# Kernel optimization log

Hardware: AMD Instinct MI355X
Metric: run time of the kernel (lower is better)

The kernel has to match this reference:

```python
import jax, jax.numpy as jnp
import numpy as np
from jax import lax

B_J0 = 0.01   # config.b_j0
R_M = 1.0     # config.R_m
BETA = 1.8    # isAdapt=1 branch
GAMMA = 0.5   # config.gamma
LENS = 0.5    # config.lens
SCALE = 6.0   # config.scale
HIGHT = 0.15  # config.hight


def _gauss(x, mu, sigma):
    return jnp.exp(-(x - mu) ** 2 / (2.0 * sigma ** 2)) / jnp.sqrt(2.0 * jnp.pi) / sigma


@jax.custom_vjp
def spike_fn(x):
    return (x > 0).astype(x.dtype)

def _spike_fwd(x):
    return spike_fn(x), x

def _spike_bwd(x, g):
    # 'MG' multi-gaussian surrogate gradient from ActFun_adp.backward
    temp = (_gauss(x, 0.0, LENS) * (1.0 + HIGHT)
            - _gauss(x, LENS, SCALE * LENS) * HIGHT
            - _gauss(x, -LENS, SCALE * LENS) * HIGHT)
    return (g * temp * GAMMA,)

spike_fn.defvjp(_spike_fwd, _spike_bwd)


def setup_inputs() -> dict:
    key = jax.random.key(0)
    ks = jax.random.split(key, 20)
    B, T, I, H, O = 256, 250, 700, 128, 20
    def xav(k, shape):
        lim = jnp.sqrt(6.0 / (shape[0] + shape[1]))
        return jax.random.uniform(k, shape, jnp.float32, -lim, lim)
    def orth(k, n):
        a = jax.random.normal(k, (n, n), jnp.float32)
        q, r = jnp.linalg.qr(a)
        return q * jnp.sign(jnp.diag(r))[None, :]
    return {
        'input': jax.random.normal(ks[0], (B, T, I), jnp.float32),
        'A1_mask': jnp.ones((H, H), jnp.float32),
        'A2_mask': jnp.ones((H, H), jnp.float32),
        'W_ih1': xav(ks[1], (H, I)), 'b_ih1': jnp.zeros((H,), jnp.float32),
        'W_h1h1': orth(ks[2], H), 'b_h1h1': jnp.zeros((H,), jnp.float32),
        'W_h1h2': xav(ks[3], (H, H)), 'b_h1h2': jnp.zeros((H,), jnp.float32),
        'W_h2h2': orth(ks[4], H), 'b_h2h2': jnp.zeros((H,), jnp.float32),
        'W_h2o': xav(ks[5], (O, H)), 'b_h2o': jnp.zeros((O,), jnp.float32),
        'tau_adp_h1': 150.0 + 10.0 * jax.random.normal(ks[6], (H,), jnp.float32),
        'tau_adp_h2': 150.0 + 10.0 * jax.random.normal(ks[7], (H,), jnp.float32),
        'tau_m_h1': 20.0 + 5.0 * jax.random.normal(ks[8], (H,), jnp.float32),
        'tau_m_h2': 20.0 + 5.0 * jax.random.normal(ks[9], (H,), jnp.float32),
        'tau_m_o': 20.0 + 5.0 * jax.random.normal(ks[10], (O,), jnp.float32),
        'hid1_mem0': jax.random.uniform(ks[11], (B, H), jnp.float32),
        'hid2_mem0': jax.random.uniform(ks[12], (B, H), jnp.float32),
        'out_mem0': jax.random.uniform(ks[13], (B, O), jnp.float32),
    }


def reference(input, A1_mask, A2_mask,
              W_ih1, b_ih1, W_h1h1, b_h1h1, W_h1h2, b_h1h2,
              W_h2h2, b_h2h2, W_h2o, b_h2o,
              tau_adp_h1, tau_adp_h2, tau_m_h1, tau_m_h2, tau_m_o,
              hid1_mem0, hid2_mem0, out_mem0):
    B, T, _ = input.shape
    H = W_ih1.shape[0]
    O = W_h2o.shape[0]
    # time-constant decays (dt = 1), computed once
    a1 = jnp.exp(-1.0 / tau_m_h1)
    r1 = jnp.exp(-1.0 / tau_adp_h1)
    a2 = jnp.exp(-1.0 / tau_m_h2)
    r2 = jnp.exp(-1.0 / tau_adp_h2)
    ao = jnp.exp(-1.0 / tau_m_o)

    xT = jnp.swapaxes(input, 0, 1)  # [T, B, I]
    carry0 = (hid1_mem0, jnp.zeros((B, H), input.dtype), jnp.full((B, H), B_J0, input.dtype),
              hid2_mem0, jnp.zeros((B, H), input.dtype), jnp.full((B, H), B_J0, input.dtype),
              out_mem0, jnp.zeros((B, O), input.dtype))

    def step(carry, xs):
        x_t, t = xs
        h1m, h1s, b1, h2m, h2s, b2, om, acc = carry
        # layer 1: input + recurrent drive, adaptive threshold LIF update
        in1 = x_t @ W_ih1.T + b_ih1 + h1s @ W_h1h1.T + b_h1h1
        b1 = r1 * b1 + (1.0 - r1) * h1s
        Bth1 = B_J0 + BETA * b1
        h1m = h1m * a1 + (1.0 - a1) * R_M * in1 - Bth1 * h1s
        h1s = spike_fn(h1m - Bth1)
        # layer 2
        in2 = h1s @ W_h1h2.T + b_h1h2 + h2s @ W_h2h2.T + b_h2h2
        b2 = r2 * b2 + (1.0 - r2) * h2s
        Bth2 = B_J0 + BETA * b2
        h2m = h2m * a2 + (1.0 - a2) * R_M * in2 - Bth2 * h2s
        h2s = spike_fn(h2m - Bth2)
        # leaky-integrator readout (no spike)
        om = om * ao + (1.0 - ao) * R_M * (h2s @ W_h2o.T + b_h2o)
        # accumulate softmax only for t > 10
        acc = acc + jnp.where(t > 10, 1.0, 0.0) * jax.nn.softmax(om, axis=1)
        return (h1m, h1s, b1, h2m, h2s, b2, om, acc), None

    final, _ = lax.scan(step, carry0, (xT, jnp.arange(T)))
    output = final[-1]
    A_norm = jnp.sum(jnp.abs(W_h1h1)) + jnp.sum(jnp.abs(W_h2h2))
    return output, A_norm


if __name__ == '__main__':
    out = reference(**setup_inputs())
    print(out[0].shape, out[1])
```

## Files before the change

### kernel.cpp

```cpp
#include <hip/hip_runtime.h>
#include <hip/hip_bf16.h>
#include <stdint.h>

#define HN 128
#define TSTEPS 250
#define ON 20
#define GK 700
#define NKT 22
#define KS 4
#define NSLOT 63

typedef _Float16 h2 __attribute__((ext_vector_type(2)));
typedef _Float16 h8 __attribute__((ext_vector_type(8)));
typedef float f4 __attribute__((ext_vector_type(4)));

__device__ __forceinline__ uint32_t pack2u(float x, float y) {
    h2 p; p.x = (_Float16)x; p.y = (_Float16)y;
    return __builtin_bit_cast(uint32_t, p);
}

__global__ __launch_bounds__(256) void ff_gemm(const float* __restrict__ X,
                                               const float* __restrict__ W,
                                               const float* __restrict__ bias,
                                               float* __restrict__ out) {
    __shared__ __align__(16) uint32_t Xs[2][128][16];
    __shared__ __align__(16) uint32_t Ws[2][128][16];
    const int tid   = threadIdx.x;
    const int w     = tid >> 6;
    const int lane  = tid & 63;
    const int m0    = blockIdx.x * 128;
    const int srow  = tid & 127;
    const int shalf = tid >> 7;
    const int lr    = lane & 15;
    const int lg    = lane >> 4;

    f4 acc[2][8];
#pragma unroll
    for (int m = 0; m < 2; ++m)
#pragma unroll
        for (int n = 0; n < 8; ++n) acc[m][n] = (f4){0.f, 0.f, 0.f, 0.f};

    float4 x4[4], w4[4];

#define LOADT(t)                                                               \
    {                                                                          \
        const int k0 = (t) * 32 + shalf * 16;                                  \
        if ((t) < 21 || shalf == 0) {                                          \
            _Pragma("unroll")                                                  \
            for (int q = 0; q < 4; ++q) {                                      \
                x4[q] = *(const float4*)&X[(size_t)(m0 + srow) * GK + k0 + q * 4]; \
                w4[q] = *(const float4*)&W[(size_t)srow * GK + k0 + q * 4];    \
            }                                                                  \
        } else {                                                               \
            _Pragma("unroll")                                                  \
            for (int q = 0; q < 3; ++q) {                                      \
                x4[q] = *(const float4*)&X[(size_t)(m0 + srow) * GK + k0 + q * 4]; \
                w4[q] = *(const float4*)&W[(size_t)srow * GK + k0 + q * 4];    \
            }                                                                  \
            x4[3] = (float4){0.f, 0.f, 0.f, 0.f};                              \
            w4[3] = (float4){0.f, 0.f, 0.f, 0.f};                              \
        }                                                                      \
    }
#define STORET(buf)                                                            \
    {                                                                          \
        _Pragma("unroll")                                                      \
        for (int q = 0; q < 4; ++q) {                                          \
            Xs[buf][srow][shalf * 8 + 2 * q]     = pack2u(x4[q].x, x4[q].y);   \
            Xs[buf][srow][shalf * 8 + 2 * q + 1] = pack2u(x4[q].z, x4[q].w);   \
            Ws[buf][srow][shalf * 8 + 2 * q]     = pack2u(w4[q].x, w4[q].y);   \
            Ws[buf][srow][shalf * 8 + 2 * q + 1] = pack2u(w4[q].z, w4[q].w);   \
        }                                                                      \
    }

    LOADT(0);
    STORET(0);
    __syncthreads();
    int cur = 0;
    for (int t = 0; t < NKT; ++t) {
        if (t + 1 < NKT) LOADT(t + 1);
        h8 a[2];
#pragma unroll
        for (int m = 0; m < 2; ++m) {
            const uint4 au = *(const uint4*)&Xs[cur][w * 32 + m * 16 + lr][lg * 4];
            a[m] = __builtin_bit_cast(h8, au);
        }
#pragma unroll
        for (int n = 0; n < 8; ++n) {
            const uint4 bu = *(const uint4*)&Ws[cur][n * 16 + lr][lg * 4];
            const h8 bf = __builtin_bit_cast(h8, bu);
            acc[0][n] = __builtin_amdgcn_mfma_f32_16x16x32_f16(a[0], bf, acc[0][n], 0, 0, 0);
            acc[1][n] = __builtin_amdgcn_mfma_f32_16x16x32_f16(a[1], bf, acc[1][n], 0, 0, 0);
        }
        if (t + 1 < NKT) STORET(cur ^ 1);
        __syncthreads();
        cur ^= 1;
    }

    float bv[8];
#pragma unroll
    for (int n = 0; n < 8; ++n) bv[n] = bias[n * 16 + lr];
#pragma unroll
    for (int m = 0; m < 2; ++m)
#pragma unroll
        for (int q = 0; q < 4; ++q) {
            const size_t row = (size_t)(m0 + w * 32 + m * 16 + lg * 4 + q);
#pragma unroll
            for (int n = 0; n < 8; ++n)
                out[row * HN + n * 16 + lr] = acc[m][n][q] + bv[n];
        }
#undef LOADT
#undef STORET
}

__device__ __forceinline__ void qrow(const float* __restrict__ src,
                                     uint4 (&wq)[8], float& sc) {
    float amax = 0.f;
#pragma unroll
    for (int q = 0; q < 32; ++q) {
        float4 v = *(const float4*)&src[q * 4];
        amax = fmaxf(amax, fmaxf(fmaxf(fabsf(v.x), fabsf(v.y)),
                                 fmaxf(fabsf(v.z), fabsf(v.w))));
    }
    const float qs = (amax > 0.f) ? 127.f / amax : 0.f;
#pragma unroll
    for (int g = 0; g < 8; ++g) {
        uint32_t u[4];
#pragma unroll
        for (int e = 0; e < 4; ++e) {
            float4 v = *(const float4*)&src[g * 16 + e * 4];
            const int q0 = (int)rintf(v.x * qs), q1 = (int)rintf(v.y * qs);
            const int q2 = (int)rintf(v.z * qs), q3 = (int)rintf(v.w * qs);
            u[e] = (uint32_t)(q0 & 255) | ((uint32_t)(q1 & 255) << 8) |
                   ((uint32_t)(q2 & 255) << 16) | ((uint32_t)(q3 & 255) << 24);
        }
        wq[g].x = u[0]; wq[g].y = u[1]; wq[g].z = u[2]; wq[g].w = u[3];
    }
    sc = (amax > 0.f) ? amax / 127.f : 0.f;
}

__device__ __forceinline__ int mvqr(const uint4 (&wq)[8], const uint4 (&sv)[8]) {
    int a0 = 0, a1 = 0, a2 = 0, a3 = 0;
#pragma unroll
    for (int g = 0; g < 8; ++g) {
        a0 = __builtin_amdgcn_sdot4((int)wq[g].x, (int)sv[g].x, a0, false);
        a1 = __builtin_amdgcn_sdot4((int)wq[g].y, (int)sv[g].y, a1, false);
        a2 = __builtin_amdgcn_sdot4((int)wq[g].z, (int)sv[g].z, a2, false);
        a3 = __builtin_amdgcn_sdot4((int)wq[g].w, (int)sv[g].w, a3, false);
    }
    return (a0 + a1) + (a2 + a3);
}

#define LOADQP(ptr, sv)                                                        \
    {                                                                          \
        const uint4* _p = (const uint4*)(ptr);                                 \
        _Pragma("unroll") for (int _g = 0; _g < 8; ++_g) sv[_g] = _p[_g];      \
    }

__device__ __forceinline__ uint32_t nib2bytes(uint32_t nib) {
    return ((nib & 15u) * 0x00204081u) & 0x01010101u;
}

__device__ __forceinline__ void spread_masks(unsigned long long lo,
                                             unsigned long long hi,
                                             uint4 (&sv)[8]) {
#pragma unroll
    for (int g = 0; g < 8; ++g) {
        const unsigned long long src = (g < 4) ? lo : hi;
        const int base = (g & 3) * 16;
        sv[g].x = nib2bytes((uint32_t)(src >> (base + 0)));
        sv[g].y = nib2bytes((uint32_t)(src >> (base + 4)));
        sv[g].z = nib2bytes((uint32_t)(src >> (base + 8)));
        sv[g].w = nib2bytes((uint32_t)(src >> (base + 12)));
    }
}

__global__ __launch_bounds__(320) void srnn_pipe13(
    const float* __restrict__ ff,
    const float* __restrict__ W_h1h1, const float* __restrict__ b_h1h1,
    const float* __restrict__ W_h1h2, const float* __restrict__ b_h1h2,
    const float* __restrict__ W_h2h2, const float* __restrict__ b_h2h2,
    const float* __restrict__ W_h2o,  const float* __restrict__ b_h2o,
    const float* __restrict__ tau_adp_h1, const float* __restrict__ tau_adp_h2,
    const float* __restrict__ tau_m_h1,   const float* __restrict__ tau_m_h2,
    const float* __restrict__ tau_m_o,
    const float* __restrict__ h1m0, const float* __restrict__ h2m0,
    const float* __restrict__ om0,
    float* __restrict__ out) {
    const int b    = blockIdx.x;
    const int tid  = threadIdx.x;
    const int w    = tid >> 6;
    const int lane = tid & 63;

    __shared__ __align__(16) uint32_t s1buf[2][KS][32];
    __shared__ __align__(16) uint32_t s2buf[2][KS][32];
    __shared__ __align__(16) float    pbbuf[2][KS][HN];
    __shared__ __align__(16) float    rdbuf[2][KS][32];

    if (w == 0) {
        const int jl = lane, jh = lane + 64;
        uint4 wql[8], wqh[8]; float sAl, sAh;
        qrow(W_h1h1 + jl * HN, wql, sAl);
        qrow(W_h1h1 + jh * HN, wqh, sAh);
        float h1m_l = h1m0[b * HN + jl], h1m_h = h1m0[b * HN + jh];
        const float a1l = expf(-1.f / tau_m_h1[jl]), a1h = expf(-1.f / tau_m_h1[jh]);
        const float r1l = expf(-1.f / tau_adp_h1[jl]), r1h = expf(-1.f / tau_adp_h1[jh]);
        const float bil = b_h1h1[jl], bih = b_h1h1[jh];
        float b1l = 0.01f, b1h = 0.01f, s1l = 0.f, s1h = 0.f;
        const float* fpl = ff + (size_t)b * TSTEPS * HN + jl;
        const float* fph = ff + (size_t)b * TSTEPS * HN + jh;
        float fcl[KS], fch[KS];
#pragma unroll
        for (int k = 0; k < KS; ++k) {
            fcl[k] = fpl[(size_t)k * HN];
            fch[k] = fph[(size_t)k * HN];
        }
        unsigned long long mklo = 0ull, mkhi = 0ull;
        for (int s = 0; s < NSLOT + 4; ++s) {
            float fnl[KS], fnh[KS];
#pragma unroll
            for (int k = 0; k < KS; ++k) {
                const int t = KS * (s + 1) + k;
                fnl[k] = (t < TSTEPS) ? fpl[(size_t)t * HN] : 0.f;
                fnh[k] = (t < TSTEPS) ? fph[(size_t)t * HN] : 0.f;
            }
            if (s < NSLOT) {
#pragma unroll
                for (int k = 0; k < KS; ++k) {
                    const int t = KS * s + k;
                    if (t < TSTEPS) {
                        uint4 sv[8];
                        spread_masks(mklo, mkhi, sv);
                        const float pAl = sAl * (float)mvqr(wql, sv);
                        const float pAh = sAh * (float)mvqr(wqh, sv);
                        b1l = r1l * b1l + (1.f - r1l) * s1l;
                        b1h = r1h * b1h + (1.f - r1h) * s1h;
                        const float Btl = 0.01f + 1.8f * b1l;
                        const float Bth = 0.01f + 1.8f * b1h;
                        h1m_l = h1m_l * a1l + (1.f - a1l) * (fcl[k] + bil + pAl) - Btl * s1l;
                        h1m_h = h1m_h * a1h + (1.f - a1h) * (fch[k] + bih + pAh) - Bth * s1h;
                        const int spl = (h1m_l - Btl > 0.f) ? 1 : 0;
                        const int sph = (h1m_h - Bth > 0.f) ? 1 : 0;
                        s1l = (float)spl; s1h = (float)sph;
                        mklo = __ballot(spl); mkhi = __ballot(sph);
                        if (lane < 32) {
                            const unsigned long long src = (lane < 16) ? mklo : mkhi;
                            s1buf[s & 1][k][lane] =
                                nib2bytes((uint32_t)(src >> ((lane & 15) * 4)));
                        }
                    }
                }
            }
#pragma unroll
            for (int k = 0; k < KS; ++k) { fcl[k] = fnl[k]; fch[k] = fnh[k]; }
            __syncthreads();
        }
    } else if (w == 1) {
        const int jl = lane, jh = lane + 64;
        uint4 wql[8], wqh[8]; float sBl, sBh;
        qrow(W_h1h2 + jl * HN, wql, sBl);
        qrow(W_h1h2 + jh * HN, wqh, sBh);
        for (int s = 0; s < NSLOT + 4; ++s) {
            if (s >= 1 && s - 1 < NSLOT) {
#pragma unroll
                for (int k = 0; k < KS; ++k) {
                    const int t = KS * (s - 1) + k;
                    if (t < TSTEPS) {
                        uint4 sv[8];
                        LOADQP(&s1buf[(s - 1) & 1][k][0], sv);
                        pbbuf[s & 1][k][jl] = sBl * (float)mvqr(wql, sv);
                        pbbuf[s & 1][k][jh] = sBh * (float)mvqr(wqh, sv);
                    }
                }
            }
            __syncthreads();
        }
    } else if (w == 2) {
        const int jl = lane, jh = lane + 64;
        uint4 wql[8], wqh[8]; float sCl, sCh;
        qrow(W_h2h2 + jl * HN, wql, sCl);
        qrow(W_h2h2 + jh * HN, wqh, sCh);
        float h2m_l = h2m0[b * HN + jl], h2m_h = h2m0[b * HN + jh];
        const float a2l = expf(-1.f / tau_m_h2[jl]), a2h = expf(-1.f / tau_m_h2[jh]);
        const float r2l = expf(-1.f / tau_adp_h2[jl]), r2h = expf(-1.f / tau_adp_h2[jh]);
        const float bil = b_h1h2[jl] + b_h2h2[jl];
        const float bih = b_h1h2[jh] + b_h2h2[jh];
        float b2l = 0.01f, b2h = 0.01f, s2l = 0.f, s2h = 0.f;
        unsigned long long mklo = 0ull, mkhi = 0ull;
        for (int s = 0; s < NSLOT + 4; ++s) {
            if (s >= 2 && s - 2 < NSLOT) {
#pragma unroll
                for (int k = 0; k < KS; ++k) {
                    const int t = KS * (s - 2) + k;
                    if (t < TSTEPS) {
                        uint4 sv[8];
                        spread_masks(mklo, mkhi, sv);
                        const float pCl = sCl * (float)mvqr(wql, sv);
                        const float pCh = sCh * (float)mvqr(wqh, sv);
                        const float pBl = pbbuf[(s - 1) & 1][k][jl];
                        const float pBh = pbbuf[(s - 1) & 1][k][jh];
                        b2l = r2l * b2l + (1.f - r2l) * s2l;
                        b2h = r2h * b2h + (1.f - r2h) * s2h;
                        const float Btl = 0.01f + 1.8f * b2l;
                        const float Bth = 0.01f + 1.8f * b2h;
                        h2m_l = h2m_l * a2l + (1.f - a2l) * (pBl + pCl + bil) - Btl * s2l;
                        h2m_h = h2m_h * a2h + (1.f - a2h) * (pBh + pCh + bih) - Bth * s2h;
                        const int spl = (h2m_l - Btl > 0.f) ? 1 : 0;
                        const int sph = (h2m_h - Bth > 0.f) ? 1 : 0;
                        s2l = (float)spl; s2h = (float)sph;
                        mklo = __ballot(spl); mkhi = __ballot(sph);
                        if (lane < 32) {
                            const unsigned long long src = (lane < 16) ? mklo : mkhi;
                            s2buf[s & 1][k][lane] =
                                nib2bytes((uint32_t)(src >> ((lane & 15) * 4)));
                        }
                    }
                }
            }
            __syncthreads();
        }
    } else if (w == 3) {
        const int o = lane;
        uint4 wq[8]; float sO;
        qrow(W_h2o + (size_t)((o < ON) ? o : 0) * HN, wq, sO);
        if (o >= ON) sO = 0.f;
        for (int s = 0; s < NSLOT + 4; ++s) {
            if (s >= 3 && s - 3 < NSLOT) {
#pragma unroll
                for (int k = 0; k < KS; ++k) {
                    const int t = KS * (s - 3) + k;
                    if (t < TSTEPS) {
                        uint4 sv[8];
                        LOADQP(&s2buf[(s - 1) & 1][k][0], sv);
                        if (o < 32) rdbuf[s & 1][k][o] = sO * (float)mvqr(wq, sv);
                    }
                }
            }
            __syncthreads();
        }
    } else {
        float omv[ON], accv[ON], aov[ON], bov[ON];
#pragma unroll
        for (int k = 0; k < ON; ++k) {
            omv[k]  = om0[b * ON + k];
            aov[k]  = expf(-1.f / tau_m_o[k]);
            bov[k]  = b_h2o[k];
            accv[k] = 0.f;
        }
        for (int s = 0; s < NSLOT + 4; ++s) {
            if (s >= 4 && s - 4 < NSLOT) {
#pragma unroll
                for (int kk = 0; kk < KS; ++kk) {
                    const int t = KS * (s - 4) + kk;
                    if (t < TSTEPS) {
                        const float4* rp = (const float4*)&rdbuf[(s - 1) & 1][kk][0];
                        const float4 r0 = rp[0], r1 = rp[1], r2 = rp[2],
                                     r3 = rp[3], r4 = rp[4];
                        float rd[ON];
                        rd[0] = r0.x;  rd[1] = r0.y;  rd[2] = r0.z;  rd[3] = r0.w;
                        rd[4] = r1.x;  rd[5] = r1.y;  rd[6] = r1.z;  rd[7] = r1.w;
                        rd[8] = r2.x;  rd[9] = r2.y;  rd[10] = r2.z; rd[11] = r2.w;
                        rd[12] = r3.x; rd[13] = r3.y; rd[14] = r3.z; rd[15] = r3.w;
                        rd[16] = r4.x; rd[17] = r4.y; rd[18] = r4.z; rd[19] = r4.w;
#pragma unroll
                        for (int k = 0; k < ON; ++k)
                            omv[k] = omv[k] * aov[k] + (1.f - aov[k]) * (rd[k] + bov[k]);
                        float m0 = omv[0], m1 = omv[1], m2 = omv[2], m3 = omv[3];
#pragma unroll
                        for (int k = 4; k < ON; k += 4) {
                            m0 = fmaxf(m0, omv[k]);
                            m1 = fmaxf(m1, omv[k + 1]);
                            m2 = fmaxf(m2, omv[k + 2]);
                            m3 = fmaxf(m3, omv[k + 3]);
                        }
                        const float mx = fmaxf(fmaxf(m0, m1), fmaxf(m2, m3));
                        float e[ON];
                        float d0 = 0.f, d1 = 0.f, d2 = 0.f, d3 = 0.f;
#pragma unroll
                        for (int k = 0; k < ON; k += 4) {
                            e[k]     = __expf(omv[k] - mx);     d0 += e[k];
                            e[k + 1] = __expf(omv[k + 1] - mx); d1 += e[k + 1];
                            e[k + 2] = __expf(omv[k + 2] - mx); d2 += e[k + 2];
                            e[k + 3] = __expf(omv[k + 3] - mx); d3 += e[k + 3];
                        }
                        const float den = (d0 + d1) + (d2 + d3);
                        if (t > 10) {
                            const float rden = 1.f / den;
#pragma unroll
                            for (int k = 0; k < ON; ++k)
                                accv[k] = fmaf(e[k], rden, accv[k]);
                        }
                    }
                }
            }
            __syncthreads();
        }
        if (lane == 0) {
#pragma unroll
            for (int k = 0; k < ON; ++k) out[b * ON + k] = accv[k];
        }
    }
}

__global__ void anorm_kernel(const float* __restrict__ W1,
                             const float* __restrict__ W2,
                             float* __restrict__ out) {
    __shared__ float red[256];
    float s = 0.f;
    for (int i = threadIdx.x; i < HN * HN; i += 256)
        s += fabsf(W1[i]) + fabsf(W2[i]);
    red[threadIdx.x] = s;
    __syncthreads();
    for (int off = 128; off > 0; off >>= 1) {
        if (threadIdx.x < off) red[threadIdx.x] += red[threadIdx.x + off];
        __syncthreads();
    }
    if (threadIdx.x == 0) out[256 * ON] = red[0];
}

extern "C" void kernel_launch(void* const* d_in, const int* in_sizes, int n_in,
                              void* d_out, int out_size, void* d_ws, size_t ws_size,
                              hipStream_t stream) {
    const float* input      = (const float*)d_in[0];
    const float* W_ih1      = (const float*)d_in[3];
    const float* b_ih1      = (const float*)d_in[4];
    const float* W_h1h1     = (const float*)d_in[5];
    const float* b_h1h1     = (const float*)d_in[6];
    const float* W_h1h2     = (const float*)d_in[7];
    const float* b_h1h2     = (const float*)d_in[8];
    const float* W_h2h2     = (const float*)d_in[9];
    const float* b_h2h2     = (const float*)d_in[10];
    const float* W_h2o      = (const float*)d_in[11];
    const float* b_h2o      = (const float*)d_in[12];
    const float* tau_adp_h1 = (const float*)d_in[13];
    const float* tau_adp_h2 = (const float*)d_in[14];
    const float* tau_m_h1   = (const float*)d_in[15];
    const float* tau_m_h2   = (const float*)d_in[16];
    const float* tau_m_o    = (const float*)d_in[17];
    const float* h1m0       = (const float*)d_in[18];
    const float* h2m0       = (const float*)d_in[19];
    const float* om0        = (const float*)d_in[20];

    float* out   = (float*)d_out;
    float* ffbuf = (float*)d_ws;

    anorm_kernel<<<1, 256, 0, stream>>>(W_h1h1, W_h2h2, out);
    ff_gemm<<<500, 256, 0, stream>>>(input, W_ih1, b_ih1, ffbuf);
    srnn_pipe13<<<256, 320, 0, stream>>>(ffbuf, W_h1h1, b_h1h1, W_h1h2, b_h1h2,
                                         W_h2h2, b_h2h2, W_h2o, b_h2o,
                                         tau_adp_h1, tau_adp_h2,
                                         tau_m_h1, tau_m_h2, tau_m_o,
                                         h1m0, h2m0, om0, out);
}
```

Measured before the change: 247.1 us.

## Store feedforward activations as fp16 and move quantized recurrent weights to shared memory

The GEMM now writes its feedforward output as fp16 instead of fp32, which halves the workspace traffic between the two kernels. The recurrent kernel quantizes all four weight matrices cooperatively into LDS at startup rather than holding them in per-wave registers. The h1->h2 projection is now split across two waves, so the block grows from 5 to 6 waves. In exchange, every dot product reads its weights from LDS, and the fp16 feedforward values carry less precision.

```diff
diff --git a/kernel.cpp b/kernel.cpp
--- a/kernel.cpp
+++ b/kernel.cpp
@@ -22,7 +22,7 @@
 __global__ __launch_bounds__(256) void ff_gemm(const float* __restrict__ X,
                                                const float* __restrict__ W,
                                                const float* __restrict__ bias,
-                                               float* __restrict__ out) {
+                                               _Float16* __restrict__ out) {
     __shared__ __align__(16) uint32_t Xs[2][128][16];
     __shared__ __align__(16) uint32_t Ws[2][128][16];
     const int tid   = threadIdx.x;
@@ -106,46 +106,35 @@
             const size_t row = (size_t)(m0 + w * 32 + m * 16 + lg * 4 + q);
 #pragma unroll
             for (int n = 0; n < 8; ++n)
-                out[row * HN + n * 16 + lr] = acc[m][n][q] + bv[n];
+                out[row * HN + n * 16 + lr] = (_Float16)(acc[m][n][q] + bv[n]);
         }
 #undef LOADT
 #undef STORET
 }
 
-__device__ __forceinline__ void qrow(const float* __restrict__ src,
-                                     uint4 (&wq)[8], float& sc) {
-    float amax = 0.f;
-#pragma unroll
-    for (int q = 0; q < 32; ++q) {
-        float4 v = *(const float4*)&src[q * 4];
-        amax = fmaxf(amax, fmaxf(fmaxf(fabsf(v.x), fabsf(v.y)),
-                                 fmaxf(fabsf(v.z), fabsf(v.w))));
-    }
-    const float qs = (amax > 0.f) ? 127.f / amax : 0.f;
+__device__ __forceinline__ int mvq(const uint4 (&W)[8][HN],
+                                   const uint4 (&sv)[8], int j) {
+    int a0 = 0, a1 = 0, a2 = 0, a3 = 0;
 #pragma unroll
     for (int g = 0; g < 8; ++g) {
-        uint32_t u[4];
-#pragma unroll
-        for (int e = 0; e < 4; ++e) {
-            float4 v = *(const float4*)&src[g * 16 + e * 4];
-            const int q0 = (int)rintf(v.x * qs), q1 = (int)rintf(v.y * qs);
-            const int q2 = (int)rintf(v.z * qs), q3 = (int)rintf(v.w * qs);
-            u[e] = (uint32_t)(q0 & 255) | ((uint32_t)(q1 & 255) << 8) |
-                   ((uint32_t)(q2 & 255) << 16) | ((uint32_t)(q3 & 255) << 24);
-        }
-        wq[g].x = u[0]; wq[g].y = u[1]; wq[g].z = u[2]; wq[g].w = u[3];
-    }
-    sc = (amax > 0.f) ? amax / 127.f : 0.f;
-}
-
-__device__ __forceinline__ int mvqr(const uint4 (&wq)[8], const uint4 (&sv)[8]) {
+        const uint4 wq = W[g][j];
+        a0 = __builtin_amdgcn_sdot4((int)wq.x, (int)sv[g].x, a0, false);
+        a1 = __builtin_amdgcn_sdot4((int)wq.y, (int)sv[g].y, a1, false);
+        a2 = __builtin_amdgcn_sdot4((int)wq.z, (int)sv[g].z, a2, false);
+        a3 = __builtin_amdgcn_sdot4((int)wq.w, (int)sv[g].w, a3, false);
+    }
+    return (a0 + a1) + (a2 + a3);
+}
+__device__ __forceinline__ int mvqo(const uint4 (&W)[8][32],
+                                    const uint4 (&sv)[8], int j) {
     int a0 = 0, a1 = 0, a2 = 0, a3 = 0;
 #pragma unroll
     for (int g = 0; g < 8; ++g) {
-        a0 = __builtin_amdgcn_sdot4((int)wq[g].x, (int)sv[g].x, a0, false);
-        a1 = __builtin_amdgcn_sdot4((int)wq[g].y, (int)sv[g].y, a1, false);
-        a2 = __builtin_amdgcn_sdot4((int)wq[g].z, (int)sv[g].z, a2, false);
-        a3 = __builtin_amdgcn_sdot4((int)wq[g].w, (int)sv[g].w, a3, false);
+        const uint4 wq = W[g][j];
+        a0 = __builtin_amdgcn_sdot4((int)wq.x, (int)sv[g].x, a0, false);
+        a1 = __builtin_amdgcn_sdot4((int)wq.y, (int)sv[g].y, a1, false);
+        a2 = __builtin_amdgcn_sdot4((int)wq.z, (int)sv[g].z, a2, false);
+        a3 = __builtin_amdgcn_sdot4((int)wq.w, (int)sv[g].w, a3, false);
     }
     return (a0 + a1) + (a2 + a3);
 }
@@ -174,8 +163,8 @@
     }
 }
 
-__global__ __launch_bounds__(320) void srnn_pipe13(
-    const float* __restrict__ ff,
+__global__ __launch_bounds__(384) void srnn_pipe15(
+    const _Float16* __restrict__ ff,
     const float* __restrict__ W_h1h1, const float* __restrict__ b_h1h1,
     const float* __restrict__ W_h1h2, const float* __restrict__ b_h1h2,
     const float* __restrict__ W_h2h2, const float* __restrict__ b_h2h2,
@@ -191,37 +180,107 @@
     const int w    = tid >> 6;
     const int lane = tid & 63;
 
-    __shared__ __align__(16) uint32_t s1buf[2][KS][32];
-    __shared__ __align__(16) uint32_t s2buf[2][KS][32];
-    __shared__ __align__(16) float    pbbuf[2][KS][HN];
-    __shared__ __align__(16) float    rdbuf[2][KS][32];
+    __shared__ __align__(16) uint4 WQA[8][HN];
+    __shared__ __align__(16) uint4 WQB[8][HN];
+    __shared__ __align__(16) uint4 WQC[8][HN];
+    __shared__ __align__(16) uint4 WQO[8][32];
+    __shared__ float scA[HN], scB[HN], scC[HN], scO[32];
+    __shared__ __align__(16) uint32_t s1ring[2][KS][32];
+    __shared__ __align__(16) uint32_t s2ring[2][KS][32];
+    __shared__ __align__(16) float    pbring[2][KS][HN];
+    __shared__ __align__(16) float    rdring[2][KS][32];
+
+    {
+        const int role = tid >> 7;
+        const int j    = tid & 127;
+        const float* src = (role == 0 ? W_h1h1 : role == 1 ? W_h1h2 : W_h2h2) + j * HN;
+        float amax = 0.f;
+#pragma unroll
+        for (int q = 0; q < 32; ++q) {
+            float4 v = *(const float4*)&src[q * 4];
+            amax = fmaxf(amax, fmaxf(fmaxf(fabsf(v.x), fabsf(v.y)),
+                                     fmaxf(fabsf(v.z), fabsf(v.w))));
+        }
+        const float qs = (amax > 0.f) ? 127.f / amax : 0.f;
+#pragma unroll
+        for (int g = 0; g < 8; ++g) {
+            uint32_t u[4];
+#pragma unroll
+            for (int e = 0; e < 4; ++e) {
+                float4 v = *(const float4*)&src[g * 16 + e * 4];
+                const int q0 = (int)rintf(v.x * qs), q1 = (int)rintf(v.y * qs);
+                const int q2 = (int)rintf(v.z * qs), q3 = (int)rintf(v.w * qs);
+                u[e] = (uint32_t)(q0 & 255) | ((uint32_t)(q1 & 255) << 8) |
+                       ((uint32_t)(q2 & 255) << 16) | ((uint32_t)(q3 & 255) << 24);
+            }
+            uint4 w4v; w4v.x = u[0]; w4v.y = u[1]; w4v.z = u[2]; w4v.w = u[3];
+            if (role == 0) WQA[g][j] = w4v;
+            else if (role == 1) WQB[g][j] = w4v;
+            else WQC[g][j] = w4v;
+        }
+        const float os = (amax > 0.f) ? amax / 127.f : 0.f;
+        if (role == 0) scA[j] = os;
+        else if (role == 1) scB[j] = os;
+        else scC[j] = os;
+    }
+    if (tid < 32) {
+        const int j = tid;
+        const bool valid = (j < ON);
+        const float* src = W_h2o + (size_t)(valid ? j : 0) * HN;
+        float amax = 0.f;
+        if (valid) {
+#pragma unroll
+            for (int q = 0; q < 32; ++q) {
+                float4 v = *(const float4*)&src[q * 4];
+                amax = fmaxf(amax, fmaxf(fmaxf(fabsf(v.x), fabsf(v.y)),
+                                         fmaxf(fabsf(v.z), fabsf(v.w))));
+            }
+        }
+        const float qs = (valid && amax > 0.f) ? 127.f / amax : 0.f;
+#pragma unroll
+        for (int g = 0; g < 8; ++g) {
+            uint32_t u[4] = {0u, 0u, 0u, 0u};
+            if (valid) {
+#pragma unroll
+                for (int e = 0; e < 4; ++e) {
+                    float4 v = *(const float4*)&src[g * 16 + e * 4];
+                    const int q0 = (int)rintf(v.x * qs), q1 = (int)rintf(v.y * qs);
+                    const int q2 = (int)rintf(v.z * qs), q3 = (int)rintf(v.w * qs);
+                    u[e] = (uint32_t)(q0 & 255) | ((uint32_t)(q1 & 255) << 8) |
+                           ((uint32_t)(q2 & 255) << 16) | ((uint32_t)(q3 & 255) << 24);
+                }
+            }
+            uint4 w4v; w4v.x = u[0]; w4v.y = u[1]; w4v.z = u[2]; w4v.w = u[3];
+            WQO[g][j] = w4v;
+        }
+        scO[j] = (valid && amax > 0.f) ? amax / 127.f : 0.f;
+    }
+    __syncthreads();
 
     if (w == 0) {
         const int jl = lane, jh = lane + 64;
-        uint4 wql[8], wqh[8]; float sAl, sAh;
-        qrow(W_h1h1 + jl * HN, wql, sAl);
-        qrow(W_h1h1 + jh * HN, wqh, sAh);
+        const float sAl = scA[jl], sAh = scA[jh];
         float h1m_l = h1m0[b * HN + jl], h1m_h = h1m0[b * HN + jh];
         const float a1l = expf(-1.f / tau_m_h1[jl]), a1h = expf(-1.f / tau_m_h1[jh]);
         const float r1l = expf(-1.f / tau_adp_h1[jl]), r1h = expf(-1.f / tau_adp_h1[jh]);
         const float bil = b_h1h1[jl], bih = b_h1h1[jh];
         float b1l = 0.01f, b1h = 0.01f, s1l = 0.f, s1h = 0.f;
-        const float* fpl = ff + (size_t)b * TSTEPS * HN + jl;
-        const float* fph = ff + (size_t)b * TSTEPS * HN + jh;
-        float fcl[KS], fch[KS];
+        const _Float16* fpl = ff + (size_t)b * TSTEPS * HN + jl;
+        const _Float16* fph = ff + (size_t)b * TSTEPS * HN + jh;
+        float fl[KS], fh[KS];
 #pragma unroll
         for (int k = 0; k < KS; ++k) {
-            fcl[k] = fpl[(size_t)k * HN];
-            fch[k] = fph[(size_t)k * HN];
+            fl[k] = (float)fpl[(size_t)k * HN];
+            fh[k] = (float)fph[(size_t)k * HN];
         }
         unsigned long long mklo = 0ull, mkhi = 0ull;
         for (int s = 0; s < NSLOT + 4; ++s) {
-            float fnl[KS], fnh[KS];
+            float nl[KS], nh[KS];
 #pragma unroll
             for (int k = 0; k < KS; ++k) {
                 const int t = KS * (s + 1) + k;
-                fnl[k] = (t < TSTEPS) ? fpl[(size_t)t * HN] : 0.f;
-                fnh[k] = (t < TSTEPS) ? fph[(size_t)t * HN] : 0.f;
+                nl[k] = (t < TSTEPS) ? (float)fpl[(size_t)t * HN] : 0.f;
+                nh[k] = (t < TSTEPS) ? (float)fph[(size_t)t * HN] : 0.f;
             }
             if (s < NSLOT) {
 #pragma unroll
@@ -230,35 +289,33 @@
                     if (t < TSTEPS) {
                         uint4 sv[8];
                         spread_masks(mklo, mkhi, sv);
-                        const float pAl = sAl * (float)mvqr(wql, sv);
-                        const float pAh = sAh * (float)mvqr(wqh, sv);
+                        const float pAl = sAl * (float)mvq(WQA, sv, jl);
+                        const float pAh = sAh * (float)mvq(WQA, sv, jh);
                         b1l = r1l * b1l + (1.f - r1l) * s1l;
                         b1h = r1h * b1h + (1.f - r1h) * s1h;
                         const float Btl = 0.01f + 1.8f * b1l;
                         const float Bth = 0.01f + 1.8f * b1h;
-                        h1m_l = h1m_l * a1l + (1.f - a1l) * (fcl[k] + bil + pAl) - Btl * s1l;
-                        h1m_h = h1m_h * a1h + (1.f - a1h) * (fch[k] + bih + pAh) - Bth * s1h;
+                        h1m_l = h1m_l * a1l + (1.f - a1l) * (fl[k] + bil + pAl) - Btl * s1l;
+                        h1m_h = h1m_h * a1h + (1.f - a1h) * (fh[k] + bih + pAh) - Bth * s1h;
                         const int spl = (h1m_l - Btl > 0.f) ? 1 : 0;
                         const int sph = (h1m_h - Bth > 0.f) ? 1 : 0;
                         s1l = (float)spl; s1h = (float)sph;
                         mklo = __ballot(spl); mkhi = __ballot(sph);
                         if (lane < 32) {
-                            const unsigned long long src = (lane < 16) ? mklo : mkhi;
-                            s1buf[s & 1][k][lane] =
-                                nib2bytes((uint32_t)(src >> ((lane & 15) * 4)));
+                            const unsigned long long srcm = (lane < 16) ? mklo : mkhi;
+                            s1ring[s & 1][k][lane] =
+                                nib2bytes((uint32_t)(srcm >> ((lane & 15) * 4)));
                         }
                     }
                 }
             }
 #pragma unroll
-            for (int k = 0; k < KS; ++k) { fcl[k] = fnl[k]; fch[k] = fnh[k]; }
+            for (int k = 0; k < KS; ++k) { fl[k] = nl[k]; fh[k] = nh[k]; }
             __syncthreads();
         }
-    } else if (w == 1) {
-        const int jl = lane, jh = lane + 64;
-        uint4 wql[8], wqh[8]; float sBl, sBh;
-        qrow(W_h1h2 + jl * HN, wql, sBl);
-        qrow(W_h1h2 + jh * HN, wqh, sBh);
+    } else if (w <= 2) {
+        const int j = ((w - 1) << 6) + lane;
+        const float sB = scB[j];
         for (int s = 0; s < NSLOT + 4; ++s) {
             if (s >= 1 && s - 1 < NSLOT) {
 #pragma unroll
@@ -266,19 +323,16 @@
                     const int t = KS * (s - 1) + k;
                     if (t < TSTEPS) {
                         uint4 sv[8];
-                        LOADQP(&s1buf[(s - 1) & 1][k][0], sv);
-                        pbbuf[s & 1][k][jl] = sBl * (float)mvqr(wql, sv);
-                        pbbuf[s & 1][k][jh] = sBh * (float)mvqr(wqh, sv);
+                        LOADQP(&s1ring[(s - 1) & 1][k][0], sv);
+                        pbring[s & 1][k][j] = sB * (float)mvq(WQB, sv, j);
                     }
                 }
             }
             __syncthreads();
         }
-    } else if (w == 2) {
+    } else if (w == 3) {
         const int jl = lane, jh = lane + 64;
-        uint4 wql[8], wqh[8]; float sCl, sCh;
-        qrow(W_h2h2 + jl * HN, wql, sCl);
-        qrow(W_h2h2 + jh * HN, wqh, sCh);
+        const float sCl = scC[jl], sCh = scC[jh];
         float h2m_l = h2m0[b * HN + jl], h2m_h = h2m0[b * HN + jh];
         const float a2l = expf(-1.f / tau_m_h2[jl]), a2h = expf(-1.f / tau_m_h2[jh]);
         const float r2l = expf(-1.f / tau_adp_h2[jl]), r2h = expf(-1.f / tau_adp_h2[jh]);
@@ -294,10 +348,10 @@
                     if (t < TSTEPS) {
                         uint4 sv[8];
                         spread_masks(mklo, mkhi, sv);
-                        const float pCl = sCl * (float)mvqr(wql, sv);
-                        const float pCh = sCh * (float)mvqr(wqh, sv);
-                        const float pBl = pbbuf[(s - 1) & 1][k][jl];
-                        const float pBh = pbbuf[(s - 1) & 1][k][jh];
+                        const float pCl = sCl * (float)mvq(WQC, sv, jl);
+                        const float pCh = sCh * (float)mvq(WQC, sv, jh);
+                        const float pBl = pbring[(s - 1) & 1][k][jl];
+                        const float pBh = pbring[(s - 1) & 1][k][jh];
                         b2l = r2l * b2l + (1.f - r2l) * s2l;
                         b2h = r2h * b2h + (1.f - r2h) * s2h;
                         const float Btl = 0.01f + 1.8f * b2l;
@@ -309,29 +363,27 @@
                         s2l = (float)spl; s2h = (float)sph;
                         mklo = __ballot(spl); mkhi = __ballot(sph);
                         if (lane < 32) {
-                            const unsigned long long src = (lane < 16) ? mklo : mkhi;
-                            s2buf[s & 1][k][lane] =
-                                nib2bytes((uint32_t)(src >> ((lane & 15) * 4)));
+                            const unsigned long long srcm = (lane < 16) ? mklo : mkhi;
+                            s2ring[s & 1][k][lane] =
+                                nib2bytes((uint32_t)(srcm >> ((lane & 15) * 4)));
                         }
                     }
                 }
             }
             __syncthreads();
         }
-    } else if (w == 3) {
+    } else if (w == 4) {
         const int o = lane;
-        uint4 wq[8]; float sO;
-        qrow(W_h2o + (size_t)((o < ON) ? o : 0) * HN, wq, sO);
-        if (o >= ON) sO = 0.f;
+        const float sO = (o < 32) ? scO[o] : 0.f;
         for (int s = 0; s < NSLOT + 4; ++s) {
             if (s >= 3 && s - 3 < NSLOT) {
 #pragma unroll
                 for (int k = 0; k < KS; ++k) {
                     const int t = KS * (s - 3) + k;
-                    if (t < TSTEPS) {
+                    if (t < TSTEPS && o < ON) {
                         uint4 sv[8];
-                        LOADQP(&s2buf[(s - 1) & 1][k][0], sv);
-                        if (o < 32) rdbuf[s & 1][k][o] = sO * (float)mvqr(wq, sv);
+                        LOADQP(&s2ring[(s - 1) & 1][k][0], sv);
+                        rdring[s & 1][k][o] = sO * (float)mvqo(WQO, sv, o);
                     }
                 }
             }
@@ -352,7 +404,7 @@
                 for (int kk = 0; kk < KS; ++kk) {
                     const int t = KS * (s - 4) + kk;
                     if (t < TSTEPS) {
-                        const float4* rp = (const float4*)&rdbuf[(s - 1) & 1][kk][0];
+                        const float4* rp = (const float4*)&rdring[(s - 1) & 1][kk][0];
                         const float4 r0 = rp[0], r1 = rp[1], r2 = rp[2],
                                      r3 = rp[3], r4 = rp[4];
                         float rd[ON];
@@ -440,12 +492,12 @@
     const float* h2m0       = (const float*)d_in[19];
     const float* om0        = (const float*)d_in[20];
 
-    float* out   = (float*)d_out;
-    float* ffbuf = (float*)d_ws;
+    float* out = (float*)d_out;
+    _Float16* ffbuf = (_Float16*)d_ws;
 
     anorm_kernel<<<1, 256, 0, stream>>>(W_h1h1, W_h2h2, out);
     ff_gemm<<<500, 256, 0, stream>>>(input, W_ih1, b_ih1, ffbuf);
-    srnn_pipe13<<<256, 320, 0, stream>>>(ffbuf, W_h1h1, b_h1h1, W_h1h2, b_h1h2,
+    srnn_pipe15<<<256, 384, 0, stream>>>(ffbuf, W_h1h1, b_h1h1, W_h1h2, b_h1h2,
                                          W_h2h2, b_h2h2, W_h2o, b_h2o,
                                          tau_adp_h1, tau_adp_h2,
                                          tau_m_h1, tau_m_h2, tau_m_o,
```

New measurement: 285.9 us. 1.16x slower.
